# Performance work log

Hardware: AMD Instinct MI355X
Metric: run time of the kernel (lower is better)

The kernel has to match this reference:

```python
import jax, jax.numpy as jnp
import numpy as np
from jax import lax

ALPHA = 0.98
DELTA = 2.0
R = 0.5
S = 0.025
EPS = 1e-6


def setup_inputs() -> dict:
    key = jax.random.key(0)
    # non-negative energy spectrogram [B, n_mels, T]
    x = jax.random.uniform(key, (64, 128, 4000), dtype=jnp.float32)
    return {"x": x}


def _pcen(x):
    # x: [B, C, T]; EMA smoother: smooth[0] = x[0], smooth[t] = (1-s)*smooth[t-1] + s*x[t]
    xt = jnp.moveaxis(x, -1, 0)  # [T, B, C]

    def step(carry, x_t):
        sm = (1.0 - S) * carry + S * x_t
        return sm, sm

    init = xt[0]
    _, sm_rest = lax.scan(step, init, xt[1:])  # [T-1, B, C]
    smooth = jnp.concatenate([init[None], sm_rest], axis=0)  # [T, B, C]
    smooth = jnp.moveaxis(smooth, 0, -1)  # [B, C, T]
    pcen = (x / (smooth + EPS) ** ALPHA + DELTA) ** R - DELTA ** R
    return pcen


def reference(x):
    return _pcen(x)
```

## Files before the change

kernel.cpp:

```cpp
#include <hip/hip_runtime.h>
#include <math.h>


constexpr int   TLEN  = 4000;
constexpr int   CHUNK = 16;
constexpr int   NTH   = 256;
constexpr float S_C   = 0.025f;
constexpr float A_C   = 1.0f - S_C;
constexpr float ALPHA = 0.98f;
constexpr float EPS_C = 1e-6f;
constexpr float SQRT2 = 1.41421356237309515f;

__global__ __launch_bounds__(NTH) void pcen_kernel(const float* __restrict__ x,
                                                   float* __restrict__ out) {
    const int    ch   = blockIdx.x;
    const size_t base = (size_t)ch * TLEN;
    const int    tid  = threadIdx.x;
    const int    lane = tid & 63;
    const int    wv   = tid >> 6;
    const bool   active = (tid * CHUNK < TLEN);

    float v[CHUNK];
    const float4* __restrict__ x4 = (const float4*)(x + base);
    if (active) {
#pragma unroll
        for (int q = 0; q < 4; ++q) {
            float4 r = x4[tid * 4 + q];
            v[q * 4 + 0] = r.x; v[q * 4 + 1] = r.y;
            v[q * 4 + 2] = r.z; v[q * 4 + 3] = r.w;
        }
    } else {
#pragma unroll
        for (int j = 0; j < CHUNK; ++j) v[j] = 0.0f;
    }

    float sm = 0.0f;
#pragma unroll
    for (int j = 0; j < CHUNK; ++j) {
        float b = S_C * v[j];
        if (tid == 0 && j == 0) b = v[0];
        sm = fmaf(A_C, sm, b);
    }
    float a16 = 1.0f;
#pragma unroll
    for (int i = 0; i < CHUNK; ++i) a16 *= A_C;

    float A = a16;
    float B = sm;

#pragma unroll
    for (int d = 1; d < 64; d <<= 1) {
        float Ap = __shfl_up(A, d);
        float Bp = __shfl_up(B, d);
        if (lane >= d) {
            B = fmaf(A, Bp, B);
            A = A * Ap;
        }
    }

    __shared__ float sA[4], sB[4];
    if (lane == 63) { sA[wv] = A; sB[wv] = B; }
    __syncthreads();
    float E = 0.0f;
    if (wv > 0) {
        float Bacc = sB[0];
        for (int w = 1; w < wv; ++w) Bacc = fmaf(sA[w], Bacc, sB[w]);
        E = Bacc;
    }

    float Ai = __shfl_up(A, 1);
    float Bi = __shfl_up(B, 1);
    if (lane == 0) { Ai = 1.0f; Bi = 0.0f; }
    float init = fmaf(Ai, E, Bi);

    sm = init;
#pragma unroll
    for (int j = 0; j < CHUNK; ++j) {
        float b = S_C * v[j];
        if (tid == 0 && j == 0) b = v[0];
        sm = fmaf(A_C, sm, b);
        float lg    = log2f(sm + EPS_C);
        float ratio = v[j] * exp2f(-ALPHA * lg);
        v[j] = sqrtf(ratio + 2.0f) - SQRT2;
    }

    if (active) {
        float4* __restrict__ o4 = (float4*)(out + base);
#pragma unroll
        for (int q = 0; q < 4; ++q) {
            float4 r;
            r.x = v[q * 4 + 0]; r.y = v[q * 4 + 1];
            r.z = v[q * 4 + 2]; r.w = v[q * 4 + 3];
            o4[tid * 4 + q] = r;
        }
    }
}

extern "C" void kernel_launch(void* const* d_in, const int* in_sizes, int n_in,
                              void* d_out, int out_size, void* d_ws, size_t ws_size,
                              hipStream_t stream) {
    const float* x   = (const float*)d_in[0];
    float*       out = (float*)d_out;
    const int nch = in_sizes[0] / TLEN;
    pcen_kernel<<<nch, NTH, 0, stream>>>(x, out);
}
```

Measured before the change: 237.8 us.

## Map one wavefront per channel and drop cross-wave scan and barrier

Each 64-lane wavefront now handles a whole 4000-sample channel, with 64 floats per lane, so the block-level shared-memory combine and __syncthreads are removed. The local pre-scan is restructured to combine four elements per step using precomputed powers of the decay. Fast intrinsics (__log2f, rsqrt-based sqrt) replace the precise math calls. Tradeoffs: higher register pressure (16 float4 per lane), strided per-lane float4 accesses that coalesce less well, and slightly reduced numerical accuracy.

```diff
diff --git a/kernel.cpp b/kernel.cpp
--- a/kernel.cpp
+++ b/kernel.cpp
@@ -2,52 +2,62 @@
 #include <math.h>
 
 
-constexpr int   TLEN  = 4000;
-constexpr int   CHUNK = 16;
-constexpr int   NTH   = 256;
-constexpr float S_C   = 0.025f;
-constexpr float A_C   = 1.0f - S_C;
+constexpr int   TLEN = 4000;
+constexpr int   NF4  = 1000;
+constexpr float S_C  = 0.025f;
+constexpr float A_1  = 1.0f - S_C;
+
+constexpr float fpow(float b, int n) {
+    float r = 1.0f;
+    for (int i = 0; i < n; ++i) r *= b;
+    return r;
+}
+constexpr float A_2  = fpow(A_1, 2);
+constexpr float A_3  = fpow(A_1, 3);
+constexpr float A_4  = fpow(A_1, 4);
+constexpr float A_64 = fpow(A_1, 64);
+
 constexpr float ALPHA = 0.98f;
 constexpr float EPS_C = 1e-6f;
 constexpr float SQRT2 = 1.41421356237309515f;
 
-__global__ __launch_bounds__(NTH) void pcen_kernel(const float* __restrict__ x,
+__device__ __forceinline__ float pcen_elem(float x, float sm) {
+    float t     = sm + EPS_C;
+    float p     = exp2f(-ALPHA * __log2f(t));
+    float y     = fmaf(x, p, 2.0f);
+    return y * __frsqrt_rn(y) - SQRT2;
+}
+
+__global__ __launch_bounds__(256) void pcen_kernel(const float* __restrict__ x,
                                                    float* __restrict__ out) {
-    const int    ch   = blockIdx.x;
-    const size_t base = (size_t)ch * TLEN;
-    const int    tid  = threadIdx.x;
-    const int    lane = tid & 63;
-    const int    wv   = tid >> 6;
-    const bool   active = (tid * CHUNK < TLEN);
+    const int tid  = threadIdx.x;
+    const int lane = tid & 63;
+    const int wv   = tid >> 6;
+    const int ch   = blockIdx.x * 4 + wv;
 
-    float v[CHUNK];
+    const size_t  base = (size_t)ch * TLEN;
     const float4* __restrict__ x4 = (const float4*)(x + base);
-    if (active) {
+    float4*       __restrict__ o4 = (float4*)(out + base);
+
+    float4 v[16];
 #pragma unroll
-        for (int q = 0; q < 4; ++q) {
-            float4 r = x4[tid * 4 + q];
-            v[q * 4 + 0] = r.x; v[q * 4 + 1] = r.y;
-            v[q * 4 + 2] = r.z; v[q * 4 + 3] = r.w;
-        }
-    } else {
-#pragma unroll
-        for (int j = 0; j < CHUNK; ++j) v[j] = 0.0f;
+    for (int q = 0; q < 16; ++q) {
+        int f4 = lane * 16 + q;
+        if (f4 < NF4) v[q] = x4[f4];
+        else          v[q] = make_float4(0.f, 0.f, 0.f, 0.f);
     }
 
     float sm = 0.0f;
 #pragma unroll
-    for (int j = 0; j < CHUNK; ++j) {
-        float b = S_C * v[j];
-        if (tid == 0 && j == 0) b = v[0];
-        sm = fmaf(A_C, sm, b);
+    for (int q = 0; q < 16; ++q) {
+        float4 r  = v[q];
+        float  b0 = (q == 0 && lane == 0) ? r.x : S_C * r.x;
+        float  w  = fmaf(A_3, b0, S_C * fmaf(A_2, r.y, fmaf(A_1, r.z, r.w)));
+        sm = fmaf(A_4, sm, w);
     }
-    float a16 = 1.0f;
-#pragma unroll
-    for (int i = 0; i < CHUNK; ++i) a16 *= A_C;
 
-    float A = a16;
+    float A = A_64;
     float B = sm;
-
 #pragma unroll
     for (int d = 1; d < 64; d <<= 1) {
         float Ap = __shfl_up(A, d);
@@ -57,42 +67,28 @@
             A = A * Ap;
         }
     }
-
-    __shared__ float sA[4], sB[4];
-    if (lane == 63) { sA[wv] = A; sB[wv] = B; }
-    __syncthreads();
-    float E = 0.0f;
-    if (wv > 0) {
-        float Bacc = sB[0];
-        for (int w = 1; w < wv; ++w) Bacc = fmaf(sA[w], Bacc, sB[w]);
-        E = Bacc;
-    }
-
-    float Ai = __shfl_up(A, 1);
-    float Bi = __shfl_up(B, 1);
-    if (lane == 0) { Ai = 1.0f; Bi = 0.0f; }
-    float init = fmaf(Ai, E, Bi);
+    float init = __shfl_up(B, 1);
+    if (lane == 0) init = 0.0f;
 
     sm = init;
 #pragma unroll
-    for (int j = 0; j < CHUNK; ++j) {
-        float b = S_C * v[j];
-        if (tid == 0 && j == 0) b = v[0];
-        sm = fmaf(A_C, sm, b);
-        float lg    = log2f(sm + EPS_C);
-        float ratio = v[j] * exp2f(-ALPHA * lg);
-        v[j] = sqrtf(ratio + 2.0f) - SQRT2;
-    }
+    for (int q = 0; q < 16; ++q) {
+        float4 r  = v[q];
+        float  b0 = (q == 0 && lane == 0) ? r.x : S_C * r.x;
+        float  s0 = fmaf(A_1, sm, b0);
+        float  s1 = fmaf(A_1, s0, S_C * r.y);
+        float  s2 = fmaf(A_1, s1, S_C * r.z);
+        float  s3 = fmaf(A_1, s2, S_C * r.w);
+        sm = s3;
 
-    if (active) {
-        float4* __restrict__ o4 = (float4*)(out + base);
-#pragma unroll
-        for (int q = 0; q < 4; ++q) {
-            float4 r;
-            r.x = v[q * 4 + 0]; r.y = v[q * 4 + 1];
-            r.z = v[q * 4 + 2]; r.w = v[q * 4 + 3];
-            o4[tid * 4 + q] = r;
-        }
+        float4 o;
+        o.x = pcen_elem(r.x, s0);
+        o.y = pcen_elem(r.y, s1);
+        o.z = pcen_elem(r.z, s2);
+        o.w = pcen_elem(r.w, s3);
+
+        int f4 = lane * 16 + q;
+        if (f4 < NF4) o4[f4] = o;
     }
 }
 
@@ -101,6 +97,6 @@
                               hipStream_t stream) {
     const float* x   = (const float*)d_in[0];
     float*       out = (float*)d_out;
-    const int nch = in_sizes[0] / TLEN;
-    pcen_kernel<<<nch, NTH, 0, stream>>>(x, out);
+    const int nch    = in_sizes[0] / TLEN;
+    pcen_kernel<<<nch / 4, 256, 0, stream>>>(x, out);
 }
```

After: 276.4 us. 1.16x slower.
